# Kernel optimization log

Measured on AMD Instinct MI355X. Metric: run time of the kernel, lower is better.

The kernel has to match this reference:

```python
import jax, jax.numpy as jnp
import numpy as np

N_NODES = 50000
N_EDGES = 800000
IN_CH = 128
OUT_CH = 32
HEADS = 4
NEG_SLOPE = 0.2


def setup_inputs() -> dict:
    key = jax.random.key(0)
    k = jax.random.split(key, 6)
    x = jax.random.normal(k[0], (N_NODES, IN_CH), dtype=jnp.float32)
    edge_index = jax.random.randint(k[1], (2, N_EDGES), 0, N_NODES, dtype=jnp.int32)
    # Glorot-style init for the learned parameters of GATConv
    W = jax.random.normal(k[2], (IN_CH, HEADS * OUT_CH), dtype=jnp.float32) / np.sqrt(IN_CH)
    att_src = jax.random.normal(k[3], (HEADS, OUT_CH), dtype=jnp.float32) / np.sqrt(OUT_CH)
    att_dst = jax.random.normal(k[4], (HEADS, OUT_CH), dtype=jnp.float32) / np.sqrt(OUT_CH)
    bias = jnp.zeros((HEADS * OUT_CH,), dtype=jnp.float32)
    return {"x": x, "edge_index": edge_index, "W": W,
            "att_src": att_src, "att_dst": att_dst, "bias": bias}


def reference(x, edge_index, W, att_src, att_dst, bias):
    # PyG GATConv, single layer: concat=True, add_self_loops=True, neg_slope=0.2
    N = x.shape[0]
    H, C = att_src.shape
    # add self loops (PyG default)
    loop = jnp.arange(N, dtype=edge_index.dtype)
    src = jnp.concatenate([edge_index[0], loop])  # [E+N] message sources j
    dst = jnp.concatenate([edge_index[1], loop])  # [E+N] message targets i
    # linear projection per head
    h = (x @ W).reshape(N, H, C)                  # [N,H,C]
    a_src = jnp.einsum('nhc,hc->nh', h, att_src)  # [N,H]
    a_dst = jnp.einsum('nhc,hc->nh', h, att_dst)  # [N,H]
    # edge-wise attention logits with LeakyReLU
    e = jax.nn.leaky_relu(a_src[src] + a_dst[dst], NEG_SLOPE)  # [E',H]
    # segment softmax over incoming edges of each destination node
    m = jax.ops.segment_max(e, dst, num_segments=N)            # [N,H]
    expe = jnp.exp(e - m[dst])
    denom = jax.ops.segment_sum(expe, dst, num_segments=N)     # [N,H]
    alpha = expe / denom[dst]                                  # [E',H]
    # scatter-aggregate weighted messages
    out = jax.ops.segment_sum(h[src] * alpha[:, :, None], dst, num_segments=N)  # [N,H,C]
    return out.reshape(N, H * C) + bias
```

## Files before the change

### kernel.cpp

```cpp
#include <hip/hip_runtime.h>


constexpr int N_NODES = 50000;
constexpr int N_EDGES = 800000;
constexpr int E_TOT   = N_EDGES + N_NODES;
constexpr int HC      = 128;
constexpr float NEG_SLOPE = 0.2f;
constexpr int M_TILES = N_NODES / 16;
constexpr int NB_GEMM = 512;
constexpr int NB_HIST = 512;
constexpr int SCAN_BLOCKS = (N_NODES + 1023) / 1024;

typedef short short8 __attribute__((ext_vector_type(8)));
typedef float f32x4  __attribute__((ext_vector_type(4)));

__device__ inline unsigned short f2bf(float f) {
    unsigned int u = __float_as_uint(f);
    u += 0x7FFF + ((u >> 16) & 1);
    return (unsigned short)(u >> 16);
}


__global__ __launch_bounds__(256) void gemm_hist(
    const float* __restrict__ x,
    const float* __restrict__ W,
    const float* __restrict__ att_src, const float* __restrict__ att_dst,
    const int* __restrict__ edst,
    unsigned short* __restrict__ hb,
    float* __restrict__ a_src, float* __restrict__ a_dst,
    int* __restrict__ deg, int* __restrict__ ppos)
{
    if (blockIdx.x >= NB_GEMM) {
        const int t0 = (blockIdx.x - NB_GEMM) * 256 + threadIdx.x;
        for (int e = t0; e < N_EDGES; e += NB_HIST * 256)
            ppos[e] = atomicAdd(&deg[edst[e]], 1);
        return;
    }
    const int wave = threadIdx.x >> 6;
    const int lane = threadIdx.x & 63;
    const int n0   = (wave & 1) * 64;
    const int l15  = lane & 15;
    const int quad = lane >> 4;

    short8 bfrag[4][4];
    #pragma unroll
    for (int t = 0; t < 4; ++t)
        #pragma unroll
        for (int ks = 0; ks < 4; ++ks) {
            short8 b;
            #pragma unroll
            for (int j = 0; j < 8; ++j)
                b[j] = (short)f2bf(W[(ks * 32 + quad * 8 + j) * 128 + n0 + t * 16 + l15]);
            bfrag[t][ks] = b;
        }

    float asw[4], adw[4];
    #pragma unroll
    for (int t = 0; t < 4; ++t) {
        asw[t] = att_src[n0 + t * 16 + l15];
        adw[t] = att_dst[n0 + t * 16 + l15];
    }

    for (int mt = blockIdx.x * 2 + (wave >> 1); mt < M_TILES; mt += NB_GEMM * 2) {
        const int m0 = mt * 16;
        short8 afrag[4];
        #pragma unroll
        for (int ks = 0; ks < 4; ++ks) {
            const float4 u0 = *(const float4*)&x[(size_t)(m0 + l15) * 128 + ks * 32 + quad * 8];
            const float4 u1 = *(const float4*)&x[(size_t)(m0 + l15) * 128 + ks * 32 + quad * 8 + 4];
            short8 a;
            a[0] = (short)f2bf(u0.x); a[1] = (short)f2bf(u0.y);
            a[2] = (short)f2bf(u0.z); a[3] = (short)f2bf(u0.w);
            a[4] = (short)f2bf(u1.x); a[5] = (short)f2bf(u1.y);
            a[6] = (short)f2bf(u1.z); a[7] = (short)f2bf(u1.w);
            afrag[ks] = a;
        }

        f32x4 acc[4];
        #pragma unroll
        for (int t = 0; t < 4; ++t) acc[t] = (f32x4){0.f, 0.f, 0.f, 0.f};

        #pragma unroll
        for (int ks = 0; ks < 4; ++ks)
            #pragma unroll
            for (int t = 0; t < 4; ++t)
                acc[t] = __builtin_amdgcn_mfma_f32_16x16x32_bf16(afrag[ks], bfrag[t][ks], acc[t], 0, 0, 0);

        #pragma unroll
        for (int t = 0; t < 4; ++t)
            #pragma unroll
            for (int r = 0; r < 4; ++r)
                hb[(m0 + quad * 4 + r) * 128 + n0 + t * 16 + l15] = f2bf(acc[t][r]);

        float hs[2][4] = {{0.f,0.f,0.f,0.f},{0.f,0.f,0.f,0.f}};
        float hd[2][4] = {{0.f,0.f,0.f,0.f},{0.f,0.f,0.f,0.f}};
        #pragma unroll
        for (int t = 0; t < 4; ++t)
            #pragma unroll
            for (int r = 0; r < 4; ++r) {
                hs[t >> 1][r] += acc[t][r] * asw[t];
                hd[t >> 1][r] += acc[t][r] * adw[t];
            }
        #pragma unroll
        for (int off = 1; off < 16; off <<= 1)
            #pragma unroll
            for (int g = 0; g < 2; ++g)
                #pragma unroll
                for (int r = 0; r < 4; ++r) {
                    hs[g][r] += __shfl_xor(hs[g][r], off);
                    hd[g][r] += __shfl_xor(hd[g][r], off);
                }
        if (l15 == 0) {
            const int hb0 = n0 >> 5;
            #pragma unroll
            for (int g = 0; g < 2; ++g)
                #pragma unroll
                for (int r = 0; r < 4; ++r) {
                    a_src[(m0 + quad * 4 + r) * 4 + hb0 + g] = hs[g][r];
                    a_dst[(m0 + quad * 4 + r) * 4 + hb0 + g] = hd[g][r];
                }
        }
    }
}


__global__ __launch_bounds__(1024) void scan_blocks(const int* __restrict__ deg,
                                                    int* __restrict__ partial,
                                                    int* __restrict__ bsum) {
    __shared__ int sm[1024];
    const int tid = threadIdx.x;
    const int i = blockIdx.x * 1024 + tid;
    const int v = (i < N_NODES) ? deg[i] + 1 : 0;
    sm[tid] = v; __syncthreads();
    for (int off = 1; off < 1024; off <<= 1) {
        const int t = (tid >= off) ? sm[tid - off] : 0;
        __syncthreads();
        sm[tid] += t;
        __syncthreads();
    }
    if (i < N_NODES) partial[i] = sm[tid] - v;
    if (tid == 1023) bsum[blockIdx.x] = sm[1023];
}

__global__ __launch_bounds__(64) void scan_bsum(int* __restrict__ bsum) {
    const int tid = threadIdx.x;
    const int v = (tid < SCAN_BLOCKS) ? bsum[tid] : 0;
    int s = v;
    #pragma unroll
    for (int off = 1; off < 64; off <<= 1) {
        const int t = __shfl_up(s, off);
        if (tid >= off) s += t;
    }
    if (tid < SCAN_BLOCKS) bsum[tid] = s - v;
}


__global__ __launch_bounds__(256) void scatter_fin(
    const int* __restrict__ esrc, const int* __restrict__ edst,
    const int* __restrict__ partial, const int* __restrict__ bsum,
    const int* __restrict__ ppos,
    int* __restrict__ row_st, int* __restrict__ csr_src)
{
    const int idx = blockIdx.x * 256 + threadIdx.x;
    if (idx < N_EDGES) {
        const int d = edst[idx];
        const int pos = partial[d] + bsum[d >> 10] + 1 + ppos[idx];
        csr_src[pos] = esrc[idx];
    } else if (idx < E_TOT) {
        const int i = idx - N_EDGES;
        const int r = partial[i] + bsum[i >> 10];
        row_st[i] = r;
        csr_src[r] = i;
        if (i == 0) row_st[N_NODES] = E_TOT;
    }
}


__global__ __launch_bounds__(256) void gat_agg(
    const int* __restrict__ row_start, const int* __restrict__ csr_src,
    const unsigned short* __restrict__ hb, const float* __restrict__ a_src,
    const float* __restrict__ a_dst, const float* __restrict__ bias,
    float* __restrict__ out)
{
    __shared__ float ws[4][256];
    const int wv = threadIdx.x >> 6;
    const int node = blockIdx.x * 4 + wv;
    if (node >= N_NODES) return;
    const int lane = threadIdx.x & 63;
    const int q    = lane >> 4;
    const int li   = lane & 15;
    const int ch0  = li * 8;
    const int hd   = li >> 2;
    const float4 ad4 = *(const float4*)&a_dst[node * 4];
    const int p0 = row_start[node], p1 = row_start[node + 1];

    float acc[8] = {0.f,0.f,0.f,0.f,0.f,0.f,0.f,0.f};
    float dsum = 0.f;

    for (int base = p0; base < p1; base += 64) {
        int m = p1 - base; if (m > 64) m = 64;
        int sv = 0;
        if (lane < m) {
            sv = csr_src[base + lane];
            const float4 av = *(const float4*)&a_src[sv * 4];
            float t; float4 w4;
            t = av.x + ad4.x; t = t > 0.f ? t : NEG_SLOPE * t; w4.x = __expf(t);
            t = av.y + ad4.y; t = t > 0.f ? t : NEG_SLOPE * t; w4.y = __expf(t);
            t = av.z + ad4.z; t = t > 0.f ? t : NEG_SLOPE * t; w4.z = __expf(t);
            t = av.w + ad4.w; t = t > 0.f ? t : NEG_SLOPE * t; w4.w = __expf(t);
            *(float4*)&ws[wv][lane * 4] = w4;
        }
        for (int j = 0; j < m; j += 4) {
            const int ei  = j + q;
            const int idx = ei < m ? ei : j;
            const int s   = __shfl(sv, idx);
            float w = ws[wv][idx * 4 + hd];
            if (ei >= m) w = 0.f;
            const uint4 hv = *(const uint4*)&hb[(size_t)s * 128 + ch0];
            acc[0] += w * __uint_as_float(hv.x << 16);
            acc[1] += w * __uint_as_float(hv.x & 0xFFFF0000u);
            acc[2] += w * __uint_as_float(hv.y << 16);
            acc[3] += w * __uint_as_float(hv.y & 0xFFFF0000u);
            acc[4] += w * __uint_as_float(hv.z << 16);
            acc[5] += w * __uint_as_float(hv.z & 0xFFFF0000u);
            acc[6] += w * __uint_as_float(hv.w << 16);
            acc[7] += w * __uint_as_float(hv.w & 0xFFFF0000u);
            dsum += w;
        }
    }
    #pragma unroll
    for (int off = 16; off <= 32; off <<= 1) {
        #pragma unroll
        for (int r = 0; r < 8; ++r) acc[r] += __shfl_xor(acc[r], off);
        dsum += __shfl_xor(dsum, off);
    }
    if (q == 0) {
        const float inv = 1.f / dsum;
        const float4 b0 = *(const float4*)&bias[ch0];
        const float4 b1 = *(const float4*)&bias[ch0 + 4];
        float4 o0, o1;
        o0.x = acc[0]*inv + b0.x; o0.y = acc[1]*inv + b0.y;
        o0.z = acc[2]*inv + b0.z; o0.w = acc[3]*inv + b0.w;
        o1.x = acc[4]*inv + b1.x; o1.y = acc[5]*inv + b1.y;
        o1.z = acc[6]*inv + b1.z; o1.w = acc[7]*inv + b1.w;
        *(float4*)&out[(size_t)node * HC + ch0]     = o0;
        *(float4*)&out[(size_t)node * HC + ch0 + 4] = o1;
    }
}

extern "C" void kernel_launch(void* const* d_in, const int* in_sizes, int n_in,
                              void* d_out, int out_size, void* d_ws, size_t ws_size,
                              hipStream_t stream) {
    const float* x       = (const float*)d_in[0];
    const int*   ei      = (const int*)  d_in[1];
    const float* W       = (const float*)d_in[2];
    const float* att_src = (const float*)d_in[3];
    const float* att_dst = (const float*)d_in[4];
    const float* bias    = (const float*)d_in[5];
    float* out = (float*)d_out;

    char* p = (char*)d_ws;
    unsigned short* hb  = (unsigned short*)p; p += (size_t)N_NODES * HC * 2;
    float* a_src = (float*)p; p += (size_t)N_NODES * 4 * 4;
    float* a_dst = (float*)p; p += (size_t)N_NODES * 4 * 4;
    int* csr_src = (int*)p;   p += (size_t)E_TOT * 4;
    int* partial = (int*)p;   p += N_NODES * 4;
    int* row_st  = (int*)p;   p += (N_NODES + 4) * 4;
    int* deg     = (int*)p;   p += N_NODES * 4;
    int* ppos    = (int*)p;   p += (size_t)N_EDGES * 4;
    int* bsum    = (int*)p;

    const int* esrc = ei;
    const int* edst = ei + N_EDGES;

    hipMemsetAsync(deg, 0, (size_t)N_NODES * sizeof(int), stream);

    gemm_hist  <<<NB_GEMM + NB_HIST, 256, 0, stream>>>(x, W, att_src, att_dst,
                                                       edst, hb, a_src, a_dst, deg, ppos);
    scan_blocks<<<SCAN_BLOCKS, 1024, 0, stream>>>(deg, partial, bsum);
    scan_bsum  <<<1, 64, 0, stream>>>(bsum);
    scatter_fin<<<(E_TOT + 255) / 256, 256, 0, stream>>>(esrc, edst, partial, bsum,
                                                         ppos, row_st, csr_src);
    gat_agg    <<<(N_NODES + 3) / 4, 256, 0, stream>>>(row_st, csr_src, hb, a_src,
                                                       a_dst, bias, out);
}
```

Before: 174.0 us.

## Reschedule stages: histogram with W cast, fuse GEMM with CSR scatter, widen aggregation lanes

The degree histogram now runs alone in its own kernel, which also pre-casts W to a transposed bf16 copy so the GEMM blocks load B fragments as vectors. The GEMM then runs alongside the CSR scatter in a single launch, and the block-sum scan is folded into the scatter blocks, so one launch is removed. In the aggregation kernel each lane now covers 16 channels, with 8 edges per iteration instead of 4. This raises per-lane register use and the cross-lane shuffle work, and it means the histogram no longer overlaps with the GEMM.

```diff
diff --git a/kernel.cpp b/kernel.cpp
--- a/kernel.cpp
+++ b/kernel.cpp
@@ -8,7 +8,7 @@
 constexpr float NEG_SLOPE = 0.2f;
 constexpr int M_TILES = N_NODES / 16;
 constexpr int NB_GEMM = 512;
-constexpr int NB_HIST = 512;
+constexpr int NB_SCAT = 512;
 constexpr int SCAN_BLOCKS = (N_NODES + 1023) / 1024;
 
 typedef short short8 __attribute__((ext_vector_type(8)));
@@ -21,105 +21,15 @@
 }
 
 
-__global__ __launch_bounds__(256) void gemm_hist(
-    const float* __restrict__ x,
-    const float* __restrict__ W,
-    const float* __restrict__ att_src, const float* __restrict__ att_dst,
-    const int* __restrict__ edst,
-    unsigned short* __restrict__ hb,
-    float* __restrict__ a_src, float* __restrict__ a_dst,
-    int* __restrict__ deg, int* __restrict__ ppos)
+__global__ __launch_bounds__(256) void hist_castw(
+    const int* __restrict__ edst, int* __restrict__ deg, int* __restrict__ ppos,
+    const float* __restrict__ W, unsigned short* __restrict__ wtb)
 {
-    if (blockIdx.x >= NB_GEMM) {
-        const int t0 = (blockIdx.x - NB_GEMM) * 256 + threadIdx.x;
-        for (int e = t0; e < N_EDGES; e += NB_HIST * 256)
-            ppos[e] = atomicAdd(&deg[edst[e]], 1);
-        return;
-    }
-    const int wave = threadIdx.x >> 6;
-    const int lane = threadIdx.x & 63;
-    const int n0   = (wave & 1) * 64;
-    const int l15  = lane & 15;
-    const int quad = lane >> 4;
-
-    short8 bfrag[4][4];
-    #pragma unroll
-    for (int t = 0; t < 4; ++t)
-        #pragma unroll
-        for (int ks = 0; ks < 4; ++ks) {
-            short8 b;
-            #pragma unroll
-            for (int j = 0; j < 8; ++j)
-                b[j] = (short)f2bf(W[(ks * 32 + quad * 8 + j) * 128 + n0 + t * 16 + l15]);
-            bfrag[t][ks] = b;
-        }
-
-    float asw[4], adw[4];
-    #pragma unroll
-    for (int t = 0; t < 4; ++t) {
-        asw[t] = att_src[n0 + t * 16 + l15];
-        adw[t] = att_dst[n0 + t * 16 + l15];
-    }
-
-    for (int mt = blockIdx.x * 2 + (wave >> 1); mt < M_TILES; mt += NB_GEMM * 2) {
-        const int m0 = mt * 16;
-        short8 afrag[4];
-        #pragma unroll
-        for (int ks = 0; ks < 4; ++ks) {
-            const float4 u0 = *(const float4*)&x[(size_t)(m0 + l15) * 128 + ks * 32 + quad * 8];
-            const float4 u1 = *(const float4*)&x[(size_t)(m0 + l15) * 128 + ks * 32 + quad * 8 + 4];
-            short8 a;
-            a[0] = (short)f2bf(u0.x); a[1] = (short)f2bf(u0.y);
-            a[2] = (short)f2bf(u0.z); a[3] = (short)f2bf(u0.w);
-            a[4] = (short)f2bf(u1.x); a[5] = (short)f2bf(u1.y);
-            a[6] = (short)f2bf(u1.z); a[7] = (short)f2bf(u1.w);
-            afrag[ks] = a;
-        }
-
-        f32x4 acc[4];
-        #pragma unroll
-        for (int t = 0; t < 4; ++t) acc[t] = (f32x4){0.f, 0.f, 0.f, 0.f};
-
-        #pragma unroll
-        for (int ks = 0; ks < 4; ++ks)
-            #pragma unroll
-            for (int t = 0; t < 4; ++t)
-                acc[t] = __builtin_amdgcn_mfma_f32_16x16x32_bf16(afrag[ks], bfrag[t][ks], acc[t], 0, 0, 0);
-
-        #pragma unroll
-        for (int t = 0; t < 4; ++t)
-            #pragma unroll
-            for (int r = 0; r < 4; ++r)
-                hb[(m0 + quad * 4 + r) * 128 + n0 + t * 16 + l15] = f2bf(acc[t][r]);
-
-        float hs[2][4] = {{0.f,0.f,0.f,0.f},{0.f,0.f,0.f,0.f}};
-        float hd[2][4] = {{0.f,0.f,0.f,0.f},{0.f,0.f,0.f,0.f}};
-        #pragma unroll
-        for (int t = 0; t < 4; ++t)
-            #pragma unroll
-            for (int r = 0; r < 4; ++r) {
-                hs[t >> 1][r] += acc[t][r] * asw[t];
-                hd[t >> 1][r] += acc[t][r] * adw[t];
-            }
-        #pragma unroll
-        for (int off = 1; off < 16; off <<= 1)
-            #pragma unroll
-            for (int g = 0; g < 2; ++g)
-                #pragma unroll
-                for (int r = 0; r < 4; ++r) {
-                    hs[g][r] += __shfl_xor(hs[g][r], off);
-                    hd[g][r] += __shfl_xor(hd[g][r], off);
-                }
-        if (l15 == 0) {
-            const int hb0 = n0 >> 5;
-            #pragma unroll
-            for (int g = 0; g < 2; ++g)
-                #pragma unroll
-                for (int r = 0; r < 4; ++r) {
-                    a_src[(m0 + quad * 4 + r) * 4 + hb0 + g] = hs[g][r];
-                    a_dst[(m0 + quad * 4 + r) * 4 + hb0 + g] = hd[g][r];
-                }
-        }
+    const int e = blockIdx.x * 256 + threadIdx.x;
+    ppos[e] = atomicAdd(&deg[edst[e]], 1);
+    if (e < 128 * 128) {
+        const int n = e >> 7, k = e & 127;
+        wtb[e] = f2bf(W[k * 128 + n]);
     }
 }
 
@@ -142,36 +52,125 @@
     if (tid == 1023) bsum[blockIdx.x] = sm[1023];
 }
 
-__global__ __launch_bounds__(64) void scan_bsum(int* __restrict__ bsum) {
-    const int tid = threadIdx.x;
-    const int v = (tid < SCAN_BLOCKS) ? bsum[tid] : 0;
-    int s = v;
-    #pragma unroll
-    for (int off = 1; off < 64; off <<= 1) {
-        const int t = __shfl_up(s, off);
-        if (tid >= off) s += t;
-    }
-    if (tid < SCAN_BLOCKS) bsum[tid] = s - v;
-}
-
-
-__global__ __launch_bounds__(256) void scatter_fin(
+
+__global__ __launch_bounds__(256) void gemm_scatter(
+    const float* __restrict__ x,
+    const unsigned short* __restrict__ wtb,
+    const float* __restrict__ att_src, const float* __restrict__ att_dst,
     const int* __restrict__ esrc, const int* __restrict__ edst,
     const int* __restrict__ partial, const int* __restrict__ bsum,
     const int* __restrict__ ppos,
-    int* __restrict__ row_st, int* __restrict__ csr_src)
+    int* __restrict__ row_st, int* __restrict__ csr_src,
+    unsigned short* __restrict__ hb,
+    float* __restrict__ a_src, float* __restrict__ a_dst)
 {
-    const int idx = blockIdx.x * 256 + threadIdx.x;
-    if (idx < N_EDGES) {
-        const int d = edst[idx];
-        const int pos = partial[d] + bsum[d >> 10] + 1 + ppos[idx];
-        csr_src[pos] = esrc[idx];
-    } else if (idx < E_TOT) {
-        const int i = idx - N_EDGES;
-        const int r = partial[i] + bsum[i >> 10];
-        row_st[i] = r;
-        csr_src[r] = i;
-        if (i == 0) row_st[N_NODES] = E_TOT;
+    if (blockIdx.x >= NB_GEMM) {
+        __shared__ int sb[64];
+        if (threadIdx.x < 64) {
+            const int v = (threadIdx.x < SCAN_BLOCKS) ? bsum[threadIdx.x] : 0;
+            int s = v;
+            #pragma unroll
+            for (int off = 1; off < 64; off <<= 1) {
+                const int t = __shfl_up(s, off);
+                if ((int)threadIdx.x >= off) s += t;
+            }
+            sb[threadIdx.x] = s - v;
+        }
+        __syncthreads();
+        for (int idx = (blockIdx.x - NB_GEMM) * 256 + threadIdx.x; idx < E_TOT;
+             idx += NB_SCAT * 256) {
+            if (idx < N_EDGES) {
+                const int d = edst[idx];
+                csr_src[partial[d] + sb[d >> 10] + 1 + ppos[idx]] = esrc[idx];
+            } else {
+                const int i = idx - N_EDGES;
+                const int r = partial[i] + sb[i >> 10];
+                row_st[i] = r;
+                csr_src[r] = i;
+                if (i == 0) row_st[N_NODES] = E_TOT;
+            }
+        }
+        return;
+    }
+    const int wave = threadIdx.x >> 6;
+    const int lane = threadIdx.x & 63;
+    const int n0   = (wave & 1) * 64;
+    const int l15  = lane & 15;
+    const int quad = lane >> 4;
+
+    short8 bfrag[4][4];
+    #pragma unroll
+    for (int t = 0; t < 4; ++t)
+        #pragma unroll
+        for (int ks = 0; ks < 4; ++ks)
+            bfrag[t][ks] = *(const short8*)&wtb[(n0 + t * 16 + l15) * 128 + ks * 32 + quad * 8];
+
+    float asw[4], adw[4];
+    #pragma unroll
+    for (int t = 0; t < 4; ++t) {
+        asw[t] = att_src[n0 + t * 16 + l15];
+        adw[t] = att_dst[n0 + t * 16 + l15];
+    }
+
+    for (int mt = blockIdx.x * 2 + (wave >> 1); mt < M_TILES; mt += NB_GEMM * 2) {
+        const int m0 = mt * 16;
+        short8 afrag[4];
+        #pragma unroll
+        for (int ks = 0; ks < 4; ++ks) {
+            const float4 u0 = *(const float4*)&x[(size_t)(m0 + l15) * 128 + ks * 32 + quad * 8];
+            const float4 u1 = *(const float4*)&x[(size_t)(m0 + l15) * 128 + ks * 32 + quad * 8 + 4];
+            short8 a;
+            a[0] = (short)f2bf(u0.x); a[1] = (short)f2bf(u0.y);
+            a[2] = (short)f2bf(u0.z); a[3] = (short)f2bf(u0.w);
+            a[4] = (short)f2bf(u1.x); a[5] = (short)f2bf(u1.y);
+            a[6] = (short)f2bf(u1.z); a[7] = (short)f2bf(u1.w);
+            afrag[ks] = a;
+        }
+
+        f32x4 acc[4];
+        #pragma unroll
+        for (int t = 0; t < 4; ++t) acc[t] = (f32x4){0.f, 0.f, 0.f, 0.f};
+
+        #pragma unroll
+        for (int ks = 0; ks < 4; ++ks)
+            #pragma unroll
+            for (int t = 0; t < 4; ++t)
+                acc[t] = __builtin_amdgcn_mfma_f32_16x16x32_bf16(afrag[ks], bfrag[t][ks], acc[t], 0, 0, 0);
+
+        #pragma unroll
+        for (int t = 0; t < 4; ++t)
+            #pragma unroll
+            for (int r = 0; r < 4; ++r)
+                hb[(m0 + quad * 4 + r) * 128 + n0 + t * 16 + l15] = f2bf(acc[t][r]);
+
+        float hs[2][4] = {{0.f,0.f,0.f,0.f},{0.f,0.f,0.f,0.f}};
+        float hd[2][4] = {{0.f,0.f,0.f,0.f},{0.f,0.f,0.f,0.f}};
+        #pragma unroll
+        for (int t = 0; t < 4; ++t)
+            #pragma unroll
+            for (int r = 0; r < 4; ++r) {
+                hs[t >> 1][r] += acc[t][r] * asw[t];
+                hd[t >> 1][r] += acc[t][r] * adw[t];
+            }
+        #pragma unroll
+        for (int off = 1; off < 16; off <<= 1)
+            #pragma unroll
+            for (int g = 0; g < 2; ++g)
+                #pragma unroll
+                for (int r = 0; r < 4; ++r) {
+                    hs[g][r] += __shfl_xor(hs[g][r], off);
+                    hd[g][r] += __shfl_xor(hd[g][r], off);
+                }
+        if (l15 == 0) {
+            const int hb0 = n0 >> 5;
+            #pragma unroll
+            for (int g = 0; g < 2; ++g)
+                #pragma unroll
+                for (int r = 0; r < 4; ++r) {
+                    a_src[(m0 + quad * 4 + r) * 4 + hb0 + g] = hs[g][r];
+                    a_dst[(m0 + quad * 4 + r) * 4 + hb0 + g] = hd[g][r];
+                }
+        }
     }
 }
 
@@ -187,14 +186,16 @@
     const int node = blockIdx.x * 4 + wv;
     if (node >= N_NODES) return;
     const int lane = threadIdx.x & 63;
-    const int q    = lane >> 4;
-    const int li   = lane & 15;
-    const int ch0  = li * 8;
-    const int hd   = li >> 2;
+    const int oct  = lane >> 3;
+    const int li   = lane & 7;
+    const int ch0  = li * 16;
+    const int hd   = li >> 1;
     const float4 ad4 = *(const float4*)&a_dst[node * 4];
     const int p0 = row_start[node], p1 = row_start[node + 1];
 
-    float acc[8] = {0.f,0.f,0.f,0.f,0.f,0.f,0.f,0.f};
+    float acc[16];
+    #pragma unroll
+    for (int r = 0; r < 16; ++r) acc[r] = 0.f;
     float dsum = 0.f;
 
     for (int base = p0; base < p1; base += 64) {
@@ -210,41 +211,49 @@
             t = av.w + ad4.w; t = t > 0.f ? t : NEG_SLOPE * t; w4.w = __expf(t);
             *(float4*)&ws[wv][lane * 4] = w4;
         }
-        for (int j = 0; j < m; j += 4) {
-            const int ei  = j + q;
+        for (int j = 0; j < m; j += 8) {
+            const int ei  = j + oct;
             const int idx = ei < m ? ei : j;
             const int s   = __shfl(sv, idx);
             float w = ws[wv][idx * 4 + hd];
             if (ei >= m) w = 0.f;
-            const uint4 hv = *(const uint4*)&hb[(size_t)s * 128 + ch0];
-            acc[0] += w * __uint_as_float(hv.x << 16);
-            acc[1] += w * __uint_as_float(hv.x & 0xFFFF0000u);
-            acc[2] += w * __uint_as_float(hv.y << 16);
-            acc[3] += w * __uint_as_float(hv.y & 0xFFFF0000u);
-            acc[4] += w * __uint_as_float(hv.z << 16);
-            acc[5] += w * __uint_as_float(hv.z & 0xFFFF0000u);
-            acc[6] += w * __uint_as_float(hv.w << 16);
-            acc[7] += w * __uint_as_float(hv.w & 0xFFFF0000u);
+            const uint4 h0 = *(const uint4*)&hb[(size_t)s * 128 + ch0];
+            const uint4 h1 = *(const uint4*)&hb[(size_t)s * 128 + ch0 + 8];
+            acc[0]  += w * __uint_as_float(h0.x << 16);
+            acc[1]  += w * __uint_as_float(h0.x & 0xFFFF0000u);
+            acc[2]  += w * __uint_as_float(h0.y << 16);
+            acc[3]  += w * __uint_as_float(h0.y & 0xFFFF0000u);
+            acc[4]  += w * __uint_as_float(h0.z << 16);
+            acc[5]  += w * __uint_as_float(h0.z & 0xFFFF0000u);
+            acc[6]  += w * __uint_as_float(h0.w << 16);
+            acc[7]  += w * __uint_as_float(h0.w & 0xFFFF0000u);
+            acc[8]  += w * __uint_as_float(h1.x << 16);
+            acc[9]  += w * __uint_as_float(h1.x & 0xFFFF0000u);
+            acc[10] += w * __uint_as_float(h1.y << 16);
+            acc[11] += w * __uint_as_float(h1.y & 0xFFFF0000u);
+            acc[12] += w * __uint_as_float(h1.z << 16);
+            acc[13] += w * __uint_as_float(h1.z & 0xFFFF0000u);
+            acc[14] += w * __uint_as_float(h1.w << 16);
+            acc[15] += w * __uint_as_float(h1.w & 0xFFFF0000u);
             dsum += w;
         }
     }
     #pragma unroll
-    for (int off = 16; off <= 32; off <<= 1) {
-        #pragma unroll
-        for (int r = 0; r < 8; ++r) acc[r] += __shfl_xor(acc[r], off);
+    for (int off = 8; off <= 32; off <<= 1) {
+        #pragma unroll
+        for (int r = 0; r < 16; ++r) acc[r] += __shfl_xor(acc[r], off);
         dsum += __shfl_xor(dsum, off);
     }
-    if (q == 0) {
+    if (oct == 0) {
         const float inv = 1.f / dsum;
-        const float4 b0 = *(const float4*)&bias[ch0];
-        const float4 b1 = *(const float4*)&bias[ch0 + 4];
-        float4 o0, o1;
-        o0.x = acc[0]*inv + b0.x; o0.y = acc[1]*inv + b0.y;
-        o0.z = acc[2]*inv + b0.z; o0.w = acc[3]*inv + b0.w;
-        o1.x = acc[4]*inv + b1.x; o1.y = acc[5]*inv + b1.y;
-        o1.z = acc[6]*inv + b1.z; o1.w = acc[7]*inv + b1.w;
-        *(float4*)&out[(size_t)node * HC + ch0]     = o0;
-        *(float4*)&out[(size_t)node * HC + ch0 + 4] = o1;
+        #pragma unroll
+        for (int v = 0; v < 4; ++v) {
+            const float4 b4 = *(const float4*)&bias[ch0 + v * 4];
+            float4 o;
+            o.x = acc[v*4+0]*inv + b4.x; o.y = acc[v*4+1]*inv + b4.y;
+            o.z = acc[v*4+2]*inv + b4.z; o.w = acc[v*4+3]*inv + b4.w;
+            *(float4*)&out[(size_t)node * HC + ch0 + v * 4] = o;
+        }
     }
 }
 
@@ -261,6 +270,7 @@
 
     char* p = (char*)d_ws;
     unsigned short* hb  = (unsigned short*)p; p += (size_t)N_NODES * HC * 2;
+    unsigned short* wtb = (unsigned short*)p; p += 128 * 128 * 2;
     float* a_src = (float*)p; p += (size_t)N_NODES * 4 * 4;
     float* a_dst = (float*)p; p += (size_t)N_NODES * 4 * 4;
     int* csr_src = (int*)p;   p += (size_t)E_TOT * 4;
@@ -275,12 +285,11 @@
 
     hipMemsetAsync(deg, 0, (size_t)N_NODES * sizeof(int), stream);
 
-    gemm_hist  <<<NB_GEMM + NB_HIST, 256, 0, stream>>>(x, W, att_src, att_dst,
-                                                       edst, hb, a_src, a_dst, deg, ppos);
-    scan_blocks<<<SCAN_BLOCKS, 1024, 0, stream>>>(deg, partial, bsum);
-    scan_bsum  <<<1, 64, 0, stream>>>(bsum);
-    scatter_fin<<<(E_TOT + 255) / 256, 256, 0, stream>>>(esrc, edst, partial, bsum,
-                                                         ppos, row_st, csr_src);
-    gat_agg    <<<(N_NODES + 3) / 4, 256, 0, stream>>>(row_st, csr_src, hb, a_src,
-                                                       a_dst, bias, out);
-}
+    hist_castw  <<<N_EDGES / 256, 256, 0, stream>>>(edst, deg, ppos, W, wtb);
+    scan_blocks <<<SCAN_BLOCKS, 1024, 0, stream>>>(deg, partial, bsum);
+    gemm_scatter<<<NB_GEMM + NB_SCAT, 256, 0, stream>>>(x, wtb, att_src, att_dst,
+                                                        esrc, edst, partial, bsum, ppos,
+                                                        row_st, csr_src, hb, a_src, a_dst);
+    gat_agg     <<<(N_NODES + 3) / 4, 256, 0, stream>>>(row_st, csr_src, hb, a_src,
+                                                        a_dst, bias, out);
+}
```

New measurement: 185.8 us. 6.8% more time.

## Spread GEMM tiles across CSR build kernels and shrink CSR indices to 16-bit

Applied to the files above, without the earlier changes.

Splits the projection GEMM into three tile ranges that run in spare blocks of the histogram, scan and scatter kernels. The idea is to hide the CSR construction phases behind useful MFMA work and drop a separate launch. It also folds the bsum scan into the scatter kernel, rewrites the block scan with wave shuffles, and stores csr_src and ppos as 16-bit values to halve that traffic. Node ids up to 50000 fit in an unsigned 16-bit value. ppos, however, truncates per-node counts, and the layout ties both arrays to this input size.

```diff
diff --git a/kernel.cpp b/kernel.cpp
--- a/kernel.cpp
+++ b/kernel.cpp
@@ -7,9 +7,14 @@
 constexpr int HC      = 128;
 constexpr float NEG_SLOPE = 0.2f;
 constexpr int M_TILES = N_NODES / 16;
-constexpr int NB_GEMM = 512;
-constexpr int NB_HIST = 512;
 constexpr int SCAN_BLOCKS = (N_NODES + 1023) / 1024;
+
+constexpr int TA_LO = 0,    TA_HI = 1024;
+constexpr int TB_LO = 1024, TB_HI = 1536;
+constexpr int TC_LO = 1536, TC_HI = M_TILES;
+constexpr int NB_HIST = 512, NB_GA = 512;
+constexpr int NB_GB = 256;
+constexpr int NB_SCAT = 512, NB_GC = 795;
 
 typedef short short8 __attribute__((ext_vector_type(8)));
 typedef float f32x4  __attribute__((ext_vector_type(4)));
@@ -21,26 +26,20 @@
 }
 
 
-__global__ __launch_bounds__(256) void gemm_hist(
-    const float* __restrict__ x,
-    const float* __restrict__ W,
+__device__ __forceinline__ void gemm_tiles(
+    int gb, int lo, int hi,
+    const float* __restrict__ x, const float* __restrict__ W,
     const float* __restrict__ att_src, const float* __restrict__ att_dst,
-    const int* __restrict__ edst,
     unsigned short* __restrict__ hb,
-    float* __restrict__ a_src, float* __restrict__ a_dst,
-    int* __restrict__ deg, int* __restrict__ ppos)
-{
-    if (blockIdx.x >= NB_GEMM) {
-        const int t0 = (blockIdx.x - NB_GEMM) * 256 + threadIdx.x;
-        for (int e = t0; e < N_EDGES; e += NB_HIST * 256)
-            ppos[e] = atomicAdd(&deg[edst[e]], 1);
-        return;
-    }
+    float* __restrict__ a_src, float* __restrict__ a_dst)
+{
     const int wave = threadIdx.x >> 6;
     const int lane = threadIdx.x & 63;
     const int n0   = (wave & 1) * 64;
     const int l15  = lane & 15;
     const int quad = lane >> 4;
+    const int mt   = lo + gb * 2 + (wave >> 1);
+    if (mt >= hi) return;
 
     short8 bfrag[4][4];
     #pragma unroll
@@ -61,123 +60,177 @@
         adw[t] = att_dst[n0 + t * 16 + l15];
     }
 
-    for (int mt = blockIdx.x * 2 + (wave >> 1); mt < M_TILES; mt += NB_GEMM * 2) {
-        const int m0 = mt * 16;
-        short8 afrag[4];
-        #pragma unroll
-        for (int ks = 0; ks < 4; ++ks) {
-            const float4 u0 = *(const float4*)&x[(size_t)(m0 + l15) * 128 + ks * 32 + quad * 8];
-            const float4 u1 = *(const float4*)&x[(size_t)(m0 + l15) * 128 + ks * 32 + quad * 8 + 4];
-            short8 a;
-            a[0] = (short)f2bf(u0.x); a[1] = (short)f2bf(u0.y);
-            a[2] = (short)f2bf(u0.z); a[3] = (short)f2bf(u0.w);
-            a[4] = (short)f2bf(u1.x); a[5] = (short)f2bf(u1.y);
-            a[6] = (short)f2bf(u1.z); a[7] = (short)f2bf(u1.w);
-            afrag[ks] = a;
-        }
-
-        f32x4 acc[4];
-        #pragma unroll
-        for (int t = 0; t < 4; ++t) acc[t] = (f32x4){0.f, 0.f, 0.f, 0.f};
-
-        #pragma unroll
-        for (int ks = 0; ks < 4; ++ks)
-            #pragma unroll
-            for (int t = 0; t < 4; ++t)
-                acc[t] = __builtin_amdgcn_mfma_f32_16x16x32_bf16(afrag[ks], bfrag[t][ks], acc[t], 0, 0, 0);
-
+    const int m0 = mt * 16;
+    short8 afrag[4];
+    #pragma unroll
+    for (int ks = 0; ks < 4; ++ks) {
+        const float4 u0 = *(const float4*)&x[(size_t)(m0 + l15) * 128 + ks * 32 + quad * 8];
+        const float4 u1 = *(const float4*)&x[(size_t)(m0 + l15) * 128 + ks * 32 + quad * 8 + 4];
+        short8 a;
+        a[0] = (short)f2bf(u0.x); a[1] = (short)f2bf(u0.y);
+        a[2] = (short)f2bf(u0.z); a[3] = (short)f2bf(u0.w);
+        a[4] = (short)f2bf(u1.x); a[5] = (short)f2bf(u1.y);
+        a[6] = (short)f2bf(u1.z); a[7] = (short)f2bf(u1.w);
+        afrag[ks] = a;
+    }
+
+    f32x4 acc[4];
+    #pragma unroll
+    for (int t = 0; t < 4; ++t) acc[t] = (f32x4){0.f, 0.f, 0.f, 0.f};
+
+    #pragma unroll
+    for (int ks = 0; ks < 4; ++ks)
         #pragma unroll
         for (int t = 0; t < 4; ++t)
-            #pragma unroll
-            for (int r = 0; r < 4; ++r)
-                hb[(m0 + quad * 4 + r) * 128 + n0 + t * 16 + l15] = f2bf(acc[t][r]);
-
-        float hs[2][4] = {{0.f,0.f,0.f,0.f},{0.f,0.f,0.f,0.f}};
-        float hd[2][4] = {{0.f,0.f,0.f,0.f},{0.f,0.f,0.f,0.f}};
-        #pragma unroll
-        for (int t = 0; t < 4; ++t)
+            acc[t] = __builtin_amdgcn_mfma_f32_16x16x32_bf16(afrag[ks], bfrag[t][ks], acc[t], 0, 0, 0);
+
+    #pragma unroll
+    for (int t = 0; t < 4; ++t)
+        #pragma unroll
+        for (int r = 0; r < 4; ++r)
+            hb[(m0 + quad * 4 + r) * 128 + n0 + t * 16 + l15] = f2bf(acc[t][r]);
+
+    float hs[2][4] = {{0.f,0.f,0.f,0.f},{0.f,0.f,0.f,0.f}};
+    float hd[2][4] = {{0.f,0.f,0.f,0.f},{0.f,0.f,0.f,0.f}};
+    #pragma unroll
+    for (int t = 0; t < 4; ++t)
+        #pragma unroll
+        for (int r = 0; r < 4; ++r) {
+            hs[t >> 1][r] += acc[t][r] * asw[t];
+            hd[t >> 1][r] += acc[t][r] * adw[t];
+        }
+    #pragma unroll
+    for (int off = 1; off < 16; off <<= 1)
+        #pragma unroll
+        for (int g = 0; g < 2; ++g)
             #pragma unroll
             for (int r = 0; r < 4; ++r) {
-                hs[t >> 1][r] += acc[t][r] * asw[t];
-                hd[t >> 1][r] += acc[t][r] * adw[t];
+                hs[g][r] += __shfl_xor(hs[g][r], off);
+                hd[g][r] += __shfl_xor(hd[g][r], off);
             }
-        #pragma unroll
-        for (int off = 1; off < 16; off <<= 1)
+    if (l15 == 0) {
+        const int hb0 = n0 >> 5;
+        #pragma unroll
+        for (int g = 0; g < 2; ++g)
             #pragma unroll
-            for (int g = 0; g < 2; ++g)
-                #pragma unroll
-                for (int r = 0; r < 4; ++r) {
-                    hs[g][r] += __shfl_xor(hs[g][r], off);
-                    hd[g][r] += __shfl_xor(hd[g][r], off);
-                }
-        if (l15 == 0) {
-            const int hb0 = n0 >> 5;
-            #pragma unroll
-            for (int g = 0; g < 2; ++g)
-                #pragma unroll
-                for (int r = 0; r < 4; ++r) {
-                    a_src[(m0 + quad * 4 + r) * 4 + hb0 + g] = hs[g][r];
-                    a_dst[(m0 + quad * 4 + r) * 4 + hb0 + g] = hd[g][r];
-                }
-        }
-    }
-}
-
-
-__global__ __launch_bounds__(1024) void scan_blocks(const int* __restrict__ deg,
-                                                    int* __restrict__ partial,
-                                                    int* __restrict__ bsum) {
-    __shared__ int sm[1024];
-    const int tid = threadIdx.x;
-    const int i = blockIdx.x * 1024 + tid;
-    const int v = (i < N_NODES) ? deg[i] + 1 : 0;
-    sm[tid] = v; __syncthreads();
-    for (int off = 1; off < 1024; off <<= 1) {
-        const int t = (tid >= off) ? sm[tid - off] : 0;
+            for (int r = 0; r < 4; ++r) {
+                a_src[(m0 + quad * 4 + r) * 4 + hb0 + g] = hs[g][r];
+                a_dst[(m0 + quad * 4 + r) * 4 + hb0 + g] = hd[g][r];
+            }
+    }
+}
+
+
+__global__ __launch_bounds__(256) void hist_gemm(
+    const int* __restrict__ edst, int* __restrict__ deg,
+    unsigned short* __restrict__ ppos,
+    const float* __restrict__ x, const float* __restrict__ W,
+    const float* __restrict__ att_src, const float* __restrict__ att_dst,
+    unsigned short* __restrict__ hb,
+    float* __restrict__ a_src, float* __restrict__ a_dst)
+{
+    if (blockIdx.x < NB_HIST) {
+        for (int e = blockIdx.x * 256 + threadIdx.x; e < N_EDGES; e += NB_HIST * 256)
+            ppos[e] = (unsigned short)atomicAdd(&deg[edst[e]], 1);
+        return;
+    }
+    gemm_tiles(blockIdx.x - NB_HIST, TA_LO, TA_HI, x, W, att_src, att_dst, hb, a_src, a_dst);
+}
+
+
+__global__ __launch_bounds__(256) void scan_gemm(
+    const int* __restrict__ deg, int* __restrict__ partial, int* __restrict__ bsum,
+    const float* __restrict__ x, const float* __restrict__ W,
+    const float* __restrict__ att_src, const float* __restrict__ att_dst,
+    unsigned short* __restrict__ hb,
+    float* __restrict__ a_src, float* __restrict__ a_dst)
+{
+    if (blockIdx.x < SCAN_BLOCKS) {
+        __shared__ int wsum[4];
+        const int tid  = threadIdx.x;
+        const int lane = tid & 63;
+        const int wv   = tid >> 6;
+        const int base = blockIdx.x * 1024 + tid * 4;
+        int d0 = 0, d1 = 0, d2 = 0, d3 = 0;
+        if (base + 3 < N_NODES) {
+            const int4 v = *(const int4*)&deg[base];
+            d0 = v.x + 1; d1 = v.y + 1; d2 = v.z + 1; d3 = v.w + 1;
+        } else {
+            if (base + 0 < N_NODES) d0 = deg[base + 0] + 1;
+            if (base + 1 < N_NODES) d1 = deg[base + 1] + 1;
+            if (base + 2 < N_NODES) d2 = deg[base + 2] + 1;
+            if (base + 3 < N_NODES) d3 = deg[base + 3] + 1;
+        }
+        const int s0 = d0, s1 = s0 + d1, s2 = s1 + d2, s3 = s2 + d3;
+        int inc = s3;
+        #pragma unroll
+        for (int off = 1; off < 64; off <<= 1) {
+            const int t = __shfl_up(inc, off);
+            if (lane >= off) inc += t;
+        }
+        if (lane == 63) wsum[wv] = inc;
         __syncthreads();
-        sm[tid] += t;
-        __syncthreads();
-    }
-    if (i < N_NODES) partial[i] = sm[tid] - v;
-    if (tid == 1023) bsum[blockIdx.x] = sm[1023];
-}
-
-__global__ __launch_bounds__(64) void scan_bsum(int* __restrict__ bsum) {
-    const int tid = threadIdx.x;
-    const int v = (tid < SCAN_BLOCKS) ? bsum[tid] : 0;
-    int s = v;
-    #pragma unroll
-    for (int off = 1; off < 64; off <<= 1) {
-        const int t = __shfl_up(s, off);
-        if (tid >= off) s += t;
-    }
-    if (tid < SCAN_BLOCKS) bsum[tid] = s - v;
-}
-
-
-__global__ __launch_bounds__(256) void scatter_fin(
+        int wbase = 0;
+        for (int k = 0; k < wv; ++k) wbase += wsum[k];
+        const int tb = wbase + inc - s3;
+        if (base + 3 < N_NODES) {
+            *(int4*)&partial[base] = (int4){tb, tb + s0, tb + s1, tb + s2};
+        } else {
+            if (base + 0 < N_NODES) partial[base + 0] = tb;
+            if (base + 1 < N_NODES) partial[base + 1] = tb + s0;
+            if (base + 2 < N_NODES) partial[base + 2] = tb + s1;
+            if (base + 3 < N_NODES) partial[base + 3] = tb + s2;
+        }
+        if (tid == 255) bsum[blockIdx.x] = wbase + inc;
+        return;
+    }
+    gemm_tiles(blockIdx.x - SCAN_BLOCKS, TB_LO, TB_HI, x, W, att_src, att_dst, hb, a_src, a_dst);
+}
+
+
+__global__ __launch_bounds__(256) void scatter_gemm(
     const int* __restrict__ esrc, const int* __restrict__ edst,
     const int* __restrict__ partial, const int* __restrict__ bsum,
-    const int* __restrict__ ppos,
-    int* __restrict__ row_st, int* __restrict__ csr_src)
-{
-    const int idx = blockIdx.x * 256 + threadIdx.x;
-    if (idx < N_EDGES) {
-        const int d = edst[idx];
-        const int pos = partial[d] + bsum[d >> 10] + 1 + ppos[idx];
-        csr_src[pos] = esrc[idx];
-    } else if (idx < E_TOT) {
-        const int i = idx - N_EDGES;
-        const int r = partial[i] + bsum[i >> 10];
-        row_st[i] = r;
-        csr_src[r] = i;
-        if (i == 0) row_st[N_NODES] = E_TOT;
-    }
+    const unsigned short* __restrict__ ppos,
+    int* __restrict__ row_st, unsigned short* __restrict__ csr_src,
+    const float* __restrict__ x, const float* __restrict__ W,
+    const float* __restrict__ att_src, const float* __restrict__ att_dst,
+    unsigned short* __restrict__ hb,
+    float* __restrict__ a_src, float* __restrict__ a_dst)
+{
+    if (blockIdx.x < NB_SCAT) {
+        __shared__ int sb[64];
+        if (threadIdx.x < 64) {
+            const int v = (threadIdx.x < SCAN_BLOCKS) ? bsum[threadIdx.x] : 0;
+            int s = v;
+            #pragma unroll
+            for (int off = 1; off < 64; off <<= 1) {
+                const int t = __shfl_up(s, off);
+                if ((int)threadIdx.x >= off) s += t;
+            }
+            sb[threadIdx.x] = s - v;
+        }
+        __syncthreads();
+        for (int idx = blockIdx.x * 256 + threadIdx.x; idx < E_TOT; idx += NB_SCAT * 256) {
+            if (idx < N_EDGES) {
+                const int d = edst[idx];
+                csr_src[partial[d] + sb[d >> 10] + 1 + ppos[idx]] = (unsigned short)esrc[idx];
+            } else {
+                const int i = idx - N_EDGES;
+                const int r = partial[i] + sb[i >> 10];
+                row_st[i] = r;
+                csr_src[r] = (unsigned short)i;
+                if (i == 0) row_st[N_NODES] = E_TOT;
+            }
+        }
+        return;
+    }
+    gemm_tiles(blockIdx.x - NB_SCAT, TC_LO, TC_HI, x, W, att_src, att_dst, hb, a_src, a_dst);
 }
 
 
 __global__ __launch_bounds__(256) void gat_agg(
-    const int* __restrict__ row_start, const int* __restrict__ csr_src,
+    const int* __restrict__ row_start, const unsigned short* __restrict__ csr_src,
     const unsigned short* __restrict__ hb, const float* __restrict__ a_src,
     const float* __restrict__ a_dst, const float* __restrict__ bias,
     float* __restrict__ out)
@@ -201,7 +254,7 @@
         int m = p1 - base; if (m > 64) m = 64;
         int sv = 0;
         if (lane < m) {
-            sv = csr_src[base + lane];
+            sv = (int)csr_src[base + lane];
             const float4 av = *(const float4*)&a_src[sv * 4];
             float t; float4 w4;
             t = av.x + ad4.x; t = t > 0.f ? t : NEG_SLOPE * t; w4.x = __expf(t);
@@ -263,11 +316,11 @@
     unsigned short* hb  = (unsigned short*)p; p += (size_t)N_NODES * HC * 2;
     float* a_src = (float*)p; p += (size_t)N_NODES * 4 * 4;
     float* a_dst = (float*)p; p += (size_t)N_NODES * 4 * 4;
-    int* csr_src = (int*)p;   p += (size_t)E_TOT * 4;
+    unsigned short* csr_src = (unsigned short*)p; p += (size_t)E_TOT * 2;
+    unsigned short* ppos    = (unsigned short*)p; p += (size_t)N_EDGES * 2;
     int* partial = (int*)p;   p += N_NODES * 4;
     int* row_st  = (int*)p;   p += (N_NODES + 4) * 4;
     int* deg     = (int*)p;   p += N_NODES * 4;
-    int* ppos    = (int*)p;   p += (size_t)N_EDGES * 4;
     int* bsum    = (int*)p;
 
     const int* esrc = ei;
@@ -275,12 +328,13 @@
 
     hipMemsetAsync(deg, 0, (size_t)N_NODES * sizeof(int), stream);
 
-    gemm_hist  <<<NB_GEMM + NB_HIST, 256, 0, stream>>>(x, W, att_src, att_dst,
-                                                       edst, hb, a_src, a_dst, deg, ppos);
-    scan_blocks<<<SCAN_BLOCKS, 1024, 0, stream>>>(deg, partial, bsum);
-    scan_bsum  <<<1, 64, 0, stream>>>(bsum);
-    scatter_fin<<<(E_TOT + 255) / 256, 256, 0, stream>>>(esrc, edst, partial, bsum,
-                                                         ppos, row_st, csr_src);
-    gat_agg    <<<(N_NODES + 3) / 4, 256, 0, stream>>>(row_st, csr_src, hb, a_src,
-                                                       a_dst, bias, out);
-}
+    hist_gemm   <<<NB_HIST + NB_GA, 256, 0, stream>>>(edst, deg, ppos,
+                                                      x, W, att_src, att_dst, hb, a_src, a_dst);
+    scan_gemm   <<<SCAN_BLOCKS + NB_GB, 256, 0, stream>>>(deg, partial, bsum,
+                                                      x, W, att_src, att_dst, hb, a_src, a_dst);
+    scatter_gemm<<<NB_SCAT + NB_GC, 256, 0, stream>>>(esrc, edst, partial, bsum, ppos,
+                                                      row_st, csr_src,
+                                                      x, W, att_src, att_dst, hb, a_src, a_dst);
+    gat_agg     <<<(N_NODES + 3) / 4, 256, 0, stream>>>(row_st, csr_src, hb, a_src,
+                                                        a_dst, bias, out);
+}
```

New measurement: 183.0 us. 1.05x slower.
